# Kernel tuning notes

Measured on AMD Instinct MI355X. Metric: run time of the kernel, lower is better.

The kernel has to match this reference:

```python
import jax, jax.numpy as jnp
import numpy as np

N = 100_000   # nodes
E = 1_600_000 # edges
D = 128       # hidden/input dim
OUT = 32      # output dim
G = 512       # graphs in batch
L = 3         # conv layers


def setup_inputs() -> dict:
    key = jax.random.key(0)
    ks = jax.random.split(key, 12)
    s = 1.0 / np.sqrt(D)
    inp = {
        "x": jax.random.normal(ks[0], (N, D), jnp.float32),
        "edge_index": jax.random.randint(ks[1], (2, E), 0, N, dtype=jnp.int32),
        "batch": jnp.sort(jax.random.randint(ks[2], (N,), 0, G, dtype=jnp.int32)),
        "enc_W1": jax.random.normal(ks[3], (D, D), jnp.float32) * s,
        "enc_b1": jnp.zeros((D,), jnp.float32),
        "enc_W2": jax.random.normal(ks[4], (D, D), jnp.float32) * s,
        "enc_b2": jnp.zeros((D,), jnp.float32),
        "gcn_W": jax.random.normal(ks[5], (L, D, D), jnp.float32) * s,
        "gcn_b": jnp.zeros((L, D), jnp.float32),
        "dec_W1": jax.random.normal(ks[6], (D, D), jnp.float32) * s,
        "dec_b1": jnp.zeros((D,), jnp.float32),
        "dec_W2": jax.random.normal(ks[7], (D, OUT), jnp.float32) * s,
        "dec_b2": jnp.zeros((OUT,), jnp.float32),
        "num_graphs": G,
    }
    return inp


def reference(x, edge_index, batch, enc_W1, enc_b1, enc_W2, enc_b2,
              gcn_W, gcn_b, dec_W1, dec_b1, dec_W2, dec_b2, num_graphs):
    n = x.shape[0]
    src, dst = edge_index[0], edge_index[1]

    # ---- encoder MLP (Linear -> ReLU -> Linear -> ReLU) ----
    h = jax.nn.relu(x @ enc_W1 + enc_b1)
    h = jax.nn.relu(h @ enc_W2 + enc_b2)

    # ---- GCN normalization: D^{-1/2} (A + I) D^{-1/2}, degrees incl. self-loops ----
    deg = jax.ops.segment_sum(jnp.ones_like(src, dtype=h.dtype), dst, num_segments=n) + 1.0
    inv_sqrt = jax.lax.rsqrt(deg)           # [N]
    edge_coef = inv_sqrt[src] * inv_sqrt[dst]  # [E]
    self_coef = inv_sqrt * inv_sqrt            # [N]

    # ---- GCN conv layers ----
    for l in range(gcn_W.shape[0]):
        hw = h @ gcn_W[l]                                       # [N, D]
        msgs = hw[src] * edge_coef[:, None]                     # [E, D] gather
        agg = jax.ops.segment_sum(msgs, dst, num_segments=n)    # [N, D] scatter-add
        agg = agg + hw * self_coef[:, None]                     # self loops
        h = jax.nn.relu(agg + gcn_b[l])

    # ---- global add pool over graphs ----
    pooled = jax.ops.segment_sum(h, batch, num_segments=num_graphs)  # [G, D]

    # ---- decoder MLP ----
    out = jax.nn.relu(pooled @ dec_W1 + dec_b1)
    return out @ dec_W2 + dec_b2
```

## Files before the change

### kernel.cpp

```cpp
#include <hip/hip_runtime.h>

#define NNODES 100000
#define NEDGES 1600000
#define DIM    128
#define OUTD   32
#define NGRAPH 512

#define NBUCK2  256
#define BSHIFT  9
#define CAP     12288
#define EPB2    8192
#define SBLOCKS ((NEDGES + EPB2 - 1) / EPB2)
#define PREPBLK 160
#define NBUILD  ((NNODES + 511) / 512)
#define EBLK64  ((NNODES + 63) / 64)
#define AGGBLK  ((NNODES + 31) / 32)
#define NZERO   (NBUCK2 + NGRAPH * DIM)
#define ZBLOCKS ((NZERO + 511) / 512)

using bf16x8 = __attribute__((ext_vector_type(8))) short;
using f32x4  = __attribute__((ext_vector_type(4))) float;
using f32x2  = __attribute__((ext_vector_type(2))) float;

__device__ __forceinline__ short f2bf(float f) {
    unsigned u = __float_as_uint(f);
    unsigned r = (u + 0x7fff + ((u >> 16) & 1)) >> 16;
    return (short)r;
}
__device__ __forceinline__ float bf2f(short s) {
    return __uint_as_float(((unsigned)(unsigned short)s) << 16);
}

__device__ __forceinline__ uint2 bf8_to_fp8(bf16x8 t) {
    float f0 = bf2f(t[0]), f1 = bf2f(t[1]), f2 = bf2f(t[2]), f3 = bf2f(t[3]);
    float f4 = bf2f(t[4]), f5 = bf2f(t[5]), f6 = bf2f(t[6]), f7 = bf2f(t[7]);
    uint2 o;
    o.x = __builtin_amdgcn_cvt_pk_fp8_f32(f0, f1, 0, false);
    o.x = __builtin_amdgcn_cvt_pk_fp8_f32(f2, f3, o.x, true);
    o.y = __builtin_amdgcn_cvt_pk_fp8_f32(f4, f5, 0, false);
    o.y = __builtin_amdgcn_cvt_pk_fp8_f32(f6, f7, o.y, true);
    return o;
}

__global__ __launch_bounds__(512) void k_zero(int* __restrict__ gz)
{
    int idx = blockIdx.x * 512 + threadIdx.x;
    if (idx < NZERO) gz[idx] = 0;
}

__global__ __launch_bounds__(512) void k_scatter_prep(
    const int* __restrict__ src, const int* __restrict__ dst,
    int* __restrict__ gcur, unsigned* __restrict__ tmp,
    const float* __restrict__ eW1, const float* __restrict__ eW2,
    const float* __restrict__ gW, short* __restrict__ WT)
{
    const int tid = threadIdx.x;

    if (blockIdx.x >= SBLOCKS) {
        int idx = (blockIdx.x - SBLOCKS) * 512 + tid;
        int mat = idx >> 14, rem = idx & 16383;
        int k = rem >> 7, n = rem & 127;
        const float* sp = (mat == 0) ? eW1 : (mat == 1) ? eW2
                                           : (gW + (size_t)(mat - 2) * 16384);
        WT[(size_t)mat * 16384 + n * DIM + k] = f2bf(sp[k * DIM + n]);
        return;
    }

    __shared__ unsigned short rnk[EPB2];
    __shared__ int h[NBUCK2];
    __shared__ int gbase[NBUCK2];
    const int base = blockIdx.x * EPB2;
    if (tid < NBUCK2) h[tid] = 0;
    __syncthreads();
    #pragma unroll
    for (int it = 0; it < EPB2 / 512; ++it) {
        int e = base + it * 512 + tid;
        if (e < NEDGES) {
            int b = dst[e] >> BSHIFT;
            rnk[it * 512 + tid] = (unsigned short)atomicAdd(&h[b], 1);
        }
    }
    __syncthreads();
    if (tid < NBUCK2 && h[tid] > 0)
        gbase[tid] = tid * CAP + atomicAdd(&gcur[tid], h[tid]);
    __syncthreads();
    #pragma unroll
    for (int it = 0; it < EPB2 / 512; ++it) {
        int e = base + it * 512 + tid;
        if (e < NEDGES) {
            int d = dst[e], sv = src[e];
            int b = d >> BSHIFT;
            int pos = gbase[b] + rnk[it * 512 + tid];
            if (pos < (b + 1) * CAP)
                tmp[pos] = (unsigned)sv | ((unsigned)(d & 511) << 17);
        }
    }
}

__global__ __launch_bounds__(512, 6) void k_build_enc01(
    const unsigned* __restrict__ tmp, const int* __restrict__ gcur,
    int* __restrict__ row_off, int* __restrict__ cntA,
    float* __restrict__ inv, int* __restrict__ col,
    const float* __restrict__ x, const short* __restrict__ WT,
    const float* __restrict__ b1, const float* __restrict__ b2,
    short* __restrict__ hbuf, int M)
{
    __shared__ short As[64 * 128];
    __shared__ short Bs[128 * 128];

    const int tid = threadIdx.x;

    if (blockIdx.x < NBUILD) {
        int* hist = (int*)As;
        int* sc   = hist + 512;
        int* lcur = sc + 512;
        const int b     = blockIdx.x;
        const int tbase = b * CAP;
        const int cnt_b = min(gcur[b], CAP);
        hist[tid] = 0;
        __syncthreads();
        for (int i = tid; i < cnt_b; i += 512)
            atomicAdd(&hist[(tmp[tbase + i] >> 17) & 511], 1);
        __syncthreads();
        const int hv = hist[tid];
        sc[tid] = hv;
        __syncthreads();
        for (int off = 1; off < 512; off <<= 1) {
            int t = (tid >= off) ? sc[tid - off] : 0;
            __syncthreads();
            sc[tid] += t;
            __syncthreads();
        }
        const int start = tbase + sc[tid] - hv;
        lcur[tid] = start;
        const int node = b * 512 + tid;
        if (node < NNODES) {
            row_off[node] = start;
            cntA[node]    = hv;
            inv[node]     = rsqrtf((float)hv + 1.0f);
        }
        __syncthreads();
        for (int i = tid; i < cnt_b; i += 512) {
            unsigned t = tmp[tbase + i];
            int pos = atomicAdd(&lcur[(t >> 17) & 511], 1);
            col[pos] = (int)((t & 0x1FFFFu) << 7);
        }
        return;
    }

    const int m0 = (blockIdx.x - NBUILD) * 64;

    #pragma unroll
    for (int i = 0; i < 2; ++i) {
        int u = tid + i * 512;
        int row = u >> 4, c = u & 15;
        int gr = min(m0 + row, M - 1);
        const float4* sp = (const float4*)(x + (size_t)gr * DIM + (c << 3));
        float4 f0 = sp[0], f1 = sp[1];
        short t8[8] = { f2bf(f0.x), f2bf(f0.y), f2bf(f0.z), f2bf(f0.w),
                        f2bf(f1.x), f2bf(f1.y), f2bf(f1.z), f2bf(f1.w) };
        *(bf16x8*)&As[row * 128 + ((c ^ (row & 15)) << 3)] = *(bf16x8*)t8;
    }

    const int wave = tid >> 6, lane = tid & 63;
    const int ml = lane & 15, quad = lane >> 4;
    const int rw = wave >> 1;
    const int cw = wave & 1;

    #pragma unroll
    for (int mat = 0; mat < 2; ++mat) {
        if (mat > 0) __syncthreads();
        #pragma unroll
        for (int i = 0; i < 4; ++i) {
            int u = tid + i * 512;
            int n = u >> 4, c = u & 15;
            *(bf16x8*)&Bs[n * 128 + ((c ^ (n & 15)) << 3)] =
                *(const bf16x8*)(WT + (size_t)mat * 16384 + n * DIM + (c << 3));
        }
        __syncthreads();

        f32x4 acc[4] = {};
        const int arow = rw * 16 + ml;
        #pragma unroll
        for (int kk = 0; kk < 4; ++kk) {
            const int c = kk * 4 + quad;
            bf16x8 a = *(bf16x8*)&As[arow * 128 + ((c ^ (arow & 15)) << 3)];
            #pragma unroll
            for (int ni = 0; ni < 4; ++ni) {
                const int brow = (cw * 4 + ni) * 16 + ml;
                bf16x8 b = *(bf16x8*)&Bs[brow * 128 + ((c ^ (brow & 15)) << 3)];
                acc[ni] = __builtin_amdgcn_mfma_f32_16x16x32_bf16(a, b, acc[ni], 0, 0, 0);
            }
        }
        __syncthreads();

        #pragma unroll
        for (int ni = 0; ni < 4; ++ni) {
            const int colc = cw * 64 + ni * 16 + ml;
            const int cc = colc >> 3, w = colc & 7;
            #pragma unroll
            for (int r = 0; r < 4; ++r) {
                const int rowl = rw * 16 + quad * 4 + r;
                float v = acc[ni][r];
                v = fmaxf(v + ((mat == 0) ? b1[colc] : b2[colc]), 0.f);
                As[rowl * 128 + (((cc ^ (rowl & 15)) << 3) | w)] = f2bf(v);
            }
        }
    }
    __syncthreads();

    #pragma unroll
    for (int i = 0; i < 2; ++i) {
        int u = tid + i * 512;
        int row = u >> 4, c = u & 15;
        int gr = m0 + row;
        if (gr < M) {
            *(bf16x8*)(hbuf + (size_t)gr * DIM + (c << 3)) =
                *(bf16x8*)&As[row * 128 + ((c ^ (row & 15)) << 3)];
        }
    }
}

__global__ __launch_bounds__(512, 8) void k_enc2(
    const short* __restrict__ hbuf, const short* __restrict__ WT,
    const float* __restrict__ inv, unsigned char* __restrict__ g8)
{
    __shared__ short As[32 * 128];
    __shared__ short Bs[128 * 128];

    const int tid = threadIdx.x;
    const int m0  = blockIdx.x * 32;

    #pragma unroll
    for (int i = 0; i < 4; ++i) {
        int u = tid + i * 512;
        int n = u >> 4, c = u & 15;
        *(bf16x8*)&Bs[n * 128 + ((c ^ (n & 15)) << 3)] =
            *(const bf16x8*)(WT + n * DIM + (c << 3));
    }
    {
        int row = tid >> 4, c = tid & 15;
        *(bf16x8*)&As[row * 128 + ((c ^ (row & 15)) << 3)] =
            *(const bf16x8*)(hbuf + (size_t)(m0 + row) * DIM + (c << 3));
    }
    __syncthreads();

    const int wave = tid >> 6, lane = tid & 63;
    const int q  = lane >> 4, sl = lane & 15;
    const int mh = wave >> 2;
    const int nq = wave & 3;
    f32x4 acc[2] = {};
    #pragma unroll
    for (int kk = 0; kk < 4; ++kk) {
        const int c = kk * 4 + q;
        bf16x8 a = *(bf16x8*)&As[(mh * 16 + sl) * 128 + ((c ^ sl) << 3)];
        #pragma unroll
        for (int ni = 0; ni < 2; ++ni) {
            bf16x8 b = *(bf16x8*)&Bs[((nq * 2 + ni) * 16 + sl) * 128 + ((c ^ sl) << 3)];
            acc[ni] = __builtin_amdgcn_mfma_f32_16x16x32_bf16(a, b, acc[ni], 0, 0, 0);
        }
    }
    __syncthreads();

    #pragma unroll
    for (int ni = 0; ni < 2; ++ni) {
        const int colc = (nq * 2 + ni) * 16 + sl;
        const int cc = colc >> 3, cw = colc & 7;
        #pragma unroll
        for (int r = 0; r < 4; ++r) {
            const int rowl = mh * 16 + q * 4 + r;
            As[rowl * 128 + (((cc ^ (rowl & 15)) << 3) | cw)] =
                f2bf(acc[ni][r] * inv[m0 + rowl]);
        }
    }
    __syncthreads();

    {
        int row = tid >> 4, c = tid & 15;
        bf16x8 t = *(bf16x8*)&As[row * 128 + ((c ^ (row & 15)) << 3)];
        *(uint2*)(g8 + (size_t)(m0 + row) * DIM + (c << 3)) = bf8_to_fp8(t);
    }
}

#define GATHER_PIPELINE()                                                      \
    const int rs = row_off[node];                                              \
    const int re = rs + cntA[node];                                            \
    int j = rs;                                                                \
    {                                                                          \
        uint2 b0, b1_, b2_, b3_, b4_, b5_, b6_, b7_;                           \
        const bool hav = (j + 7 < re);                                         \
        if (hav) {                                                             \
            b0 = GLD(col[j]);     b1_ = GLD(col[j + 1]);                       \
            b2_ = GLD(col[j + 2]); b3_ = GLD(col[j + 3]);                      \
            b4_ = GLD(col[j + 4]); b5_ = GLD(col[j + 5]);                      \
            b6_ = GLD(col[j + 6]); b7_ = GLD(col[j + 7]);                      \
            j += 8;                                                            \
        }                                                                      \
        for (; j + 7 < re; j += 8) {                                           \
            uint2 n0 = GLD(col[j]);     uint2 n1 = GLD(col[j + 1]);            \
            uint2 n2 = GLD(col[j + 2]); uint2 n3 = GLD(col[j + 3]);            \
            uint2 n4 = GLD(col[j + 4]); uint2 n5 = GLD(col[j + 5]);            \
            uint2 n6 = GLD(col[j + 6]); uint2 n7 = GLD(col[j + 7]);            \
            ACC8(b0) ACC8(b1_) ACC8(b2_) ACC8(b3_)                             \
            ACC8(b4_) ACC8(b5_) ACC8(b6_) ACC8(b7_)                            \
            b0 = n0; b1_ = n1; b2_ = n2; b3_ = n3;                             \
            b4_ = n4; b5_ = n5; b6_ = n6; b7_ = n7;                            \
        }                                                                      \
        if (hav) {                                                             \
            ACC8(b0) ACC8(b1_) ACC8(b2_) ACC8(b3_)                             \
            ACC8(b4_) ACC8(b5_) ACC8(b6_) ACC8(b7_)                            \
        }                                                                      \
    }                                                                          \
    for (; j + 3 < re; j += 4) {                                               \
        uint2 v0 = GLD(col[j]);     uint2 v1 = GLD(col[j + 1]);                \
        uint2 v2 = GLD(col[j + 2]); uint2 v3 = GLD(col[j + 3]);                \
        ACC8(v0) ACC8(v1) ACC8(v2) ACC8(v3)                                    \
    }                                                                          \
    for (; j < re; ++j) {                                                      \
        uint2 v = GLD(col[j]);                                                 \
        ACC8(v)                                                                \
    }

__global__ __launch_bounds__(512, 8) void k_agg_gemm(
    const unsigned char* __restrict__ g8v, const int* __restrict__ row_off,
    const int* __restrict__ cntA, const int* __restrict__ col,
    const float* __restrict__ inv, const float* __restrict__ bias,
    const short* __restrict__ WT, unsigned char* __restrict__ g8o)
{
    __shared__ short As[32 * 128];
    __shared__ short Bs[128 * 128];

    const int tid = threadIdx.x;

    #pragma unroll
    for (int i = 0; i < 4; ++i) {
        int u = tid + i * 512;
        int n = u >> 4, c = u & 15;
        *(bf16x8*)&Bs[n * 128 + ((c ^ (n & 15)) << 3)] =
            *(const bf16x8*)(WT + n * DIM + (c << 3));
    }

    const int wave = tid >> 6, lane = tid & 63;
    const int q    = lane >> 4;
    const int sl   = lane & 15;
    const int sl8  = sl << 3;
    const int nl   = wave * 4 + q;
    const int m0   = blockIdx.x * 32;
    const int node = m0 + nl;

    f32x2 a01, a23, a45, a67;
    {
        uint2 us = *(const uint2*)(g8v + (size_t)node * 128 + sl8);
        a01 = __builtin_amdgcn_cvt_pk_f32_fp8(us.x, false);
        a23 = __builtin_amdgcn_cvt_pk_f32_fp8(us.x, true);
        a45 = __builtin_amdgcn_cvt_pk_f32_fp8(us.y, false);
        a67 = __builtin_amdgcn_cvt_pk_f32_fp8(us.y, true);
    }

    #define ACC8(v) \
        a01 += __builtin_amdgcn_cvt_pk_f32_fp8(v.x, false); \
        a23 += __builtin_amdgcn_cvt_pk_f32_fp8(v.x, true);  \
        a45 += __builtin_amdgcn_cvt_pk_f32_fp8(v.y, false); \
        a67 += __builtin_amdgcn_cvt_pk_f32_fp8(v.y, true);
    #define GLD(c) (*(const uint2*)(g8v + (size_t)(unsigned)((c) + sl8)))

    GATHER_PIPELINE()

    #undef ACC8
    #undef GLD

    const float scv = inv[node];
    const float4 bb0 = ((const float4*)bias)[sl * 2];
    const float4 bb1 = ((const float4*)bias)[sl * 2 + 1];
    short o[8];
    o[0] = f2bf(fmaxf(fmaf(a01[0], scv, bb0.x), 0.f));
    o[1] = f2bf(fmaxf(fmaf(a01[1], scv, bb0.y), 0.f));
    o[2] = f2bf(fmaxf(fmaf(a23[0], scv, bb0.z), 0.f));
    o[3] = f2bf(fmaxf(fmaf(a23[1], scv, bb0.w), 0.f));
    o[4] = f2bf(fmaxf(fmaf(a45[0], scv, bb1.x), 0.f));
    o[5] = f2bf(fmaxf(fmaf(a45[1], scv, bb1.y), 0.f));
    o[6] = f2bf(fmaxf(fmaf(a67[0], scv, bb1.z), 0.f));
    o[7] = f2bf(fmaxf(fmaf(a67[1], scv, bb1.w), 0.f));
    *(bf16x8*)&As[nl * 128 + ((sl ^ (nl & 15)) << 3)] = *(bf16x8*)o;
    __syncthreads();

    const int mh = wave >> 2;
    const int nq = wave & 3;
    f32x4 acc[2] = {};
    #pragma unroll
    for (int kk = 0; kk < 4; ++kk) {
        const int c = kk * 4 + q;
        bf16x8 a = *(bf16x8*)&As[(mh * 16 + sl) * 128 + ((c ^ sl) << 3)];
        #pragma unroll
        for (int ni = 0; ni < 2; ++ni) {
            bf16x8 b = *(bf16x8*)&Bs[((nq * 2 + ni) * 16 + sl) * 128 + ((c ^ sl) << 3)];
            acc[ni] = __builtin_amdgcn_mfma_f32_16x16x32_bf16(a, b, acc[ni], 0, 0, 0);
        }
    }
    __syncthreads();

    #pragma unroll
    for (int ni = 0; ni < 2; ++ni) {
        const int colc = (nq * 2 + ni) * 16 + sl;
        const int cc   = colc >> 3, cw = colc & 7;
        #pragma unroll
        for (int r = 0; r < 4; ++r) {
            const int rowl = mh * 16 + q * 4 + r;
            As[rowl * 128 + (((cc ^ (rowl & 15)) << 3) | cw)] =
                f2bf(acc[ni][r] * inv[m0 + rowl]);
        }
    }
    __syncthreads();

    {
        int row = tid >> 4, c = tid & 15;
        bf16x8 t = *(bf16x8*)&As[row * 128 + ((c ^ (row & 15)) << 3)];
        *(uint2*)(g8o + (size_t)(m0 + row) * DIM + (c << 3)) = bf8_to_fp8(t);
    }
}

__global__ __launch_bounds__(512) void k_agg_pool(
    const unsigned char* __restrict__ g8v, const int* __restrict__ row_off,
    const int* __restrict__ cntA, const int* __restrict__ col,
    const float* __restrict__ inv, const float* __restrict__ bias,
    const int* __restrict__ batch, float* __restrict__ pooled)
{
    __shared__ float Hs[32][132];
    __shared__ int sbatch[32];

    const int tid = threadIdx.x;
    const int wave = tid >> 6, lane = tid & 63;
    const int q    = lane >> 4;
    const int sl   = lane & 15;
    const int sl8  = sl << 3;
    const int nl   = wave * 4 + q;
    const int m0   = blockIdx.x * 32;
    const int node = m0 + nl;

    if (tid < 32) sbatch[tid] = batch[m0 + tid];

    f32x2 a01, a23, a45, a67;
    {
        uint2 us = *(const uint2*)(g8v + (size_t)node * 128 + sl8);
        a01 = __builtin_amdgcn_cvt_pk_f32_fp8(us.x, false);
        a23 = __builtin_amdgcn_cvt_pk_f32_fp8(us.x, true);
        a45 = __builtin_amdgcn_cvt_pk_f32_fp8(us.y, false);
        a67 = __builtin_amdgcn_cvt_pk_f32_fp8(us.y, true);
    }

    #define ACC8(v) \
        a01 += __builtin_amdgcn_cvt_pk_f32_fp8(v.x, false); \
        a23 += __builtin_amdgcn_cvt_pk_f32_fp8(v.x, true);  \
        a45 += __builtin_amdgcn_cvt_pk_f32_fp8(v.y, false); \
        a67 += __builtin_amdgcn_cvt_pk_f32_fp8(v.y, true);
    #define GLD(c) (*(const uint2*)(g8v + (size_t)(unsigned)((c) + sl8)))

    GATHER_PIPELINE()

    #undef ACC8
    #undef GLD

    const float scv = inv[node];
    const float4 bb0 = ((const float4*)bias)[sl * 2];
    const float4 bb1 = ((const float4*)bias)[sl * 2 + 1];
    float4 h0, h1;
    h0.x = fmaxf(fmaf(a01[0], scv, bb0.x), 0.f);
    h0.y = fmaxf(fmaf(a01[1], scv, bb0.y), 0.f);
    h0.z = fmaxf(fmaf(a23[0], scv, bb0.z), 0.f);
    h0.w = fmaxf(fmaf(a23[1], scv, bb0.w), 0.f);
    h1.x = fmaxf(fmaf(a45[0], scv, bb1.x), 0.f);
    h1.y = fmaxf(fmaf(a45[1], scv, bb1.y), 0.f);
    h1.z = fmaxf(fmaf(a67[0], scv, bb1.z), 0.f);
    h1.w = fmaxf(fmaf(a67[1], scv, bb1.w), 0.f);
    *(float4*)&Hs[nl][sl * 8]     = h0;
    *(float4*)&Hs[nl][sl * 8 + 4] = h1;
    __syncthreads();

    const int d   = tid & 127;
    const int grp = tid >> 7;
    float acc = 0.f;
    int cg = -1;
    #pragma unroll
    for (int i = 0; i < 8; ++i) {
        const int nn = grp * 8 + i;
        const int g  = sbatch[nn];
        if (g != cg) {
            if (cg >= 0) atomicAdd(pooled + (size_t)cg * DIM + d, acc);
            cg = g; acc = 0.f;
        }
        acc += Hs[nn][d];
    }
    atomicAdd(pooled + (size_t)cg * DIM + d, acc);
}

__global__ __launch_bounds__(512) void k_dec(
    const float* __restrict__ pooled, const float* __restrict__ W1,
    const float* __restrict__ b1, const float* __restrict__ W2,
    const float* __restrict__ b2, float* __restrict__ out)
{
    __shared__ float pbuf[8][128];
    __shared__ float tbuf[8][128];
    const int wave = threadIdx.x >> 6, lane = threadIdx.x & 63;
    const int g = blockIdx.x * 8 + wave;

    float2 pv = *(const float2*)(pooled + (size_t)g * DIM + lane * 2);
    pbuf[wave][lane * 2]     = pv.x;
    pbuf[wave][lane * 2 + 1] = pv.y;
    __syncthreads();

    float t0 = 0.f, t1 = 0.f;
    #pragma unroll 8
    for (int k = 0; k < DIM; ++k) {
        float pk = pbuf[wave][k];
        float2 w = *(const float2*)(W1 + (size_t)k * DIM + lane * 2);
        t0 = fmaf(pk, w.x, t0);
        t1 = fmaf(pk, w.y, t1);
    }
    tbuf[wave][lane * 2]     = fmaxf(t0 + b1[lane * 2],     0.f);
    tbuf[wave][lane * 2 + 1] = fmaxf(t1 + b1[lane * 2 + 1], 0.f);
    __syncthreads();

    const int c = lane & 31, hh = lane >> 5;
    float part = 0.f;
    #pragma unroll 8
    for (int kk = 0; kk < 64; ++kk) {
        int k = hh * 64 + kk;
        part = fmaf(tbuf[wave][k], W2[(size_t)k * OUTD + c], part);
    }
    float other = __shfl_xor(part, 32, 64);
    if (hh == 0)
        out[(size_t)g * OUTD + c] = part + other + b2[c];
}

extern "C" void kernel_launch(void* const* d_in, const int* in_sizes, int n_in,
                              void* d_out, int out_size, void* d_ws, size_t ws_size,
                              hipStream_t stream)
{
    const float* x      = (const float*)d_in[0];
    const int*   ei     = (const int*)d_in[1];
    const int*   batch  = (const int*)d_in[2];
    const float* enc_W1 = (const float*)d_in[3];
    const float* enc_b1 = (const float*)d_in[4];
    const float* enc_W2 = (const float*)d_in[5];
    const float* enc_b2 = (const float*)d_in[6];
    const float* gcn_W  = (const float*)d_in[7];
    const float* gcn_b  = (const float*)d_in[8];
    const float* dec_W1 = (const float*)d_in[9];
    const float* dec_b1 = (const float*)d_in[10];
    const float* dec_W2 = (const float*)d_in[11];
    const float* dec_b2 = (const float*)d_in[12];
    float* out = (float*)d_out;

    const int* src = ei;
    const int* dst = ei + NEDGES;

    char* p = (char*)d_ws;
    auto alloc = [&](size_t bytes) -> void* {
        void* r = (void*)p;
        p += (bytes + 255) & ~(size_t)255;
        return r;
    };
    int*           gcur   = (int*)          alloc((size_t)NBUCK2 * sizeof(int));
    float*         pooled = (float*)        alloc((size_t)NGRAPH * DIM * sizeof(float));
    unsigned char* g8a    = (unsigned char*)alloc((size_t)NNODES * DIM);
    unsigned char* g8b    = (unsigned char*)alloc((size_t)NNODES * DIM);
    short*         hbuf   = (short*)        alloc((size_t)NNODES * DIM * sizeof(short));
    float*         inv    = (float*)        alloc((size_t)NNODES * sizeof(float));
    int*           row_off= (int*)          alloc((size_t)NNODES * sizeof(int));
    int*           cntA   = (int*)          alloc((size_t)NNODES * sizeof(int));
    int*           col    = (int*)          alloc((size_t)NBUCK2 * CAP * sizeof(int));
    unsigned*      tmp    = (unsigned*)     alloc((size_t)NBUCK2 * CAP * sizeof(unsigned));
    short*         WT     = (short*)        alloc((size_t)5 * DIM * DIM * sizeof(short));

    k_zero<<<ZBLOCKS, 512, 0, stream>>>(gcur);

    k_scatter_prep<<<SBLOCKS + PREPBLK, 512, 0, stream>>>(
        src, dst, gcur, tmp, enc_W1, enc_W2, gcn_W, WT);

    k_build_enc01<<<NBUILD + EBLK64, 512, 0, stream>>>(
        tmp, gcur, row_off, cntA, inv, col,
        x, WT, enc_b1, enc_b2, hbuf, NNODES);

    k_enc2<<<AGGBLK, 512, 0, stream>>>(hbuf, WT + 2 * 16384, inv, g8a);

    k_agg_gemm<<<AGGBLK, 512, 0, stream>>>(g8a, row_off, cntA, col, inv,
                                           gcn_b,       WT + 3 * 16384, g8b);
    k_agg_gemm<<<AGGBLK, 512, 0, stream>>>(g8b, row_off, cntA, col, inv,
                                           gcn_b + 128, WT + 4 * 16384, g8a);
    k_agg_pool<<<AGGBLK, 512, 0, stream>>>(g8a, row_off, cntA, col, inv,
                                           gcn_b + 256, batch, pooled);

    k_dec <<<NGRAPH / 8, 512, 0, stream>>>(pooled, dec_W1, dec_b1,
                                           dec_W2, dec_b2, out);
}
```

Baseline: 293.5 us.

## Enlarge enc2 GEMM tile to 128 rows and cache dst in LDS during scatter

The second encoder GEMM now processes 128 rows per block instead of 32, so the 32 KB bf16 weight tile loaded into LDS is reused across four times as many rows. Each wave computes a 4x2 grid of MFMA tiles, and the tail block is handled with clamped loads and guarded stores. The scatter-prep kernel halves its edges per block and keeps each dst value in shared memory, so the second pass no longer reloads dst from global memory. In exchange there are fewer, larger enc2 blocks with more LDS and more accumulator registers per block, and twice as many scatter blocks contending on the global bucket counters.

After: 293.9 us. Within noise of the previous version (+0.1%).

```diff
diff --git a/kernel.cpp b/kernel.cpp
--- a/kernel.cpp
+++ b/kernel.cpp
@@ -9,11 +9,12 @@
 #define NBUCK2  256
 #define BSHIFT  9
 #define CAP     12288
-#define EPB2    8192
+#define EPB2    4096
 #define SBLOCKS ((NEDGES + EPB2 - 1) / EPB2)
 #define PREPBLK 160
 #define NBUILD  ((NNODES + 511) / 512)
 #define EBLK64  ((NNODES + 63) / 64)
+#define EBLK128 ((NNODES + 127) / 128)
 #define AGGBLK  ((NNODES + 31) / 32)
 #define NZERO   (NBUCK2 + NGRAPH * DIM)
 #define ZBLOCKS ((NZERO + 511) / 512)
@@ -67,6 +68,7 @@
     }
 
     __shared__ unsigned short rnk[EPB2];
+    __shared__ unsigned       eds[EPB2];
     __shared__ int h[NBUCK2];
     __shared__ int gbase[NBUCK2];
     const int base = blockIdx.x * EPB2;
@@ -76,8 +78,9 @@
     for (int it = 0; it < EPB2 / 512; ++it) {
         int e = base + it * 512 + tid;
         if (e < NEDGES) {
-            int b = dst[e] >> BSHIFT;
-            rnk[it * 512 + tid] = (unsigned short)atomicAdd(&h[b], 1);
+            unsigned d = (unsigned)dst[e];
+            eds[it * 512 + tid] = d;
+            rnk[it * 512 + tid] = (unsigned short)atomicAdd(&h[d >> BSHIFT], 1);
         }
     }
     __syncthreads();
@@ -88,11 +91,12 @@
     for (int it = 0; it < EPB2 / 512; ++it) {
         int e = base + it * 512 + tid;
         if (e < NEDGES) {
-            int d = dst[e], sv = src[e];
+            unsigned d = eds[it * 512 + tid];
+            int sv = src[e];
             int b = d >> BSHIFT;
             int pos = gbase[b] + rnk[it * 512 + tid];
             if (pos < (b + 1) * CAP)
-                tmp[pos] = (unsigned)sv | ((unsigned)(d & 511) << 17);
+                tmp[pos] = (unsigned)sv | ((d & 511) << 17);
         }
     }
 }
@@ -221,15 +225,15 @@
     }
 }
 
-__global__ __launch_bounds__(512, 8) void k_enc2(
+__global__ __launch_bounds__(512, 4) void k_enc2(
     const short* __restrict__ hbuf, const short* __restrict__ WT,
-    const float* __restrict__ inv, unsigned char* __restrict__ g8)
-{
-    __shared__ short As[32 * 128];
+    const float* __restrict__ inv, unsigned char* __restrict__ g8, int M)
+{
+    __shared__ short As[128 * 128];
     __shared__ short Bs[128 * 128];
 
     const int tid = threadIdx.x;
-    const int m0  = blockIdx.x * 32;
+    const int m0  = blockIdx.x * 128;
 
     #pragma unroll
     for (int i = 0; i < 4; ++i) {
@@ -238,10 +242,13 @@
         *(bf16x8*)&Bs[n * 128 + ((c ^ (n & 15)) << 3)] =
             *(const bf16x8*)(WT + n * DIM + (c << 3));
     }
-    {
-        int row = tid >> 4, c = tid & 15;
+    #pragma unroll
+    for (int i = 0; i < 4; ++i) {
+        int u = tid + i * 512;
+        int row = u >> 4, c = u & 15;
+        int gr = min(m0 + row, M - 1);
         *(bf16x8*)&As[row * 128 + ((c ^ (row & 15)) << 3)] =
-            *(const bf16x8*)(hbuf + (size_t)(m0 + row) * DIM + (c << 3));
+            *(const bf16x8*)(hbuf + (size_t)gr * DIM + (c << 3));
     }
     __syncthreads();
 
@@ -249,36 +256,47 @@
     const int q  = lane >> 4, sl = lane & 15;
     const int mh = wave >> 2;
     const int nq = wave & 3;
-    f32x4 acc[2] = {};
+    f32x4 acc[4][2] = {};
     #pragma unroll
     for (int kk = 0; kk < 4; ++kk) {
         const int c = kk * 4 + q;
-        bf16x8 a = *(bf16x8*)&As[(mh * 16 + sl) * 128 + ((c ^ sl) << 3)];
+        bf16x8 b0 = *(bf16x8*)&Bs[((nq * 2 + 0) * 16 + sl) * 128 + ((c ^ sl) << 3)];
+        bf16x8 b1v = *(bf16x8*)&Bs[((nq * 2 + 1) * 16 + sl) * 128 + ((c ^ sl) << 3)];
+        #pragma unroll
+        for (int r4 = 0; r4 < 4; ++r4) {
+            const int arow = (mh * 4 + r4) * 16 + sl;
+            bf16x8 a = *(bf16x8*)&As[arow * 128 + ((c ^ sl) << 3)];
+            acc[r4][0] = __builtin_amdgcn_mfma_f32_16x16x32_bf16(a, b0, acc[r4][0], 0, 0, 0);
+            acc[r4][1] = __builtin_amdgcn_mfma_f32_16x16x32_bf16(a, b1v, acc[r4][1], 0, 0, 0);
+        }
+    }
+    __syncthreads();
+
+    #pragma unroll
+    for (int r4 = 0; r4 < 4; ++r4) {
         #pragma unroll
         for (int ni = 0; ni < 2; ++ni) {
-            bf16x8 b = *(bf16x8*)&Bs[((nq * 2 + ni) * 16 + sl) * 128 + ((c ^ sl) << 3)];
-            acc[ni] = __builtin_amdgcn_mfma_f32_16x16x32_bf16(a, b, acc[ni], 0, 0, 0);
-        }
-    }
-    __syncthreads();
-
-    #pragma unroll
-    for (int ni = 0; ni < 2; ++ni) {
-        const int colc = (nq * 2 + ni) * 16 + sl;
-        const int cc = colc >> 3, cw = colc & 7;
-        #pragma unroll
-        for (int r = 0; r < 4; ++r) {
-            const int rowl = mh * 16 + q * 4 + r;
-            As[rowl * 128 + (((cc ^ (rowl & 15)) << 3) | cw)] =
-                f2bf(acc[ni][r] * inv[m0 + rowl]);
-        }
-    }
-    __syncthreads();
-
-    {
-        int row = tid >> 4, c = tid & 15;
-        bf16x8 t = *(bf16x8*)&As[row * 128 + ((c ^ (row & 15)) << 3)];
-        *(uint2*)(g8 + (size_t)(m0 + row) * DIM + (c << 3)) = bf8_to_fp8(t);
+            const int colc = (nq * 2 + ni) * 16 + sl;
+            const int cc = colc >> 3, cw = colc & 7;
+            #pragma unroll
+            for (int r = 0; r < 4; ++r) {
+                const int rowl = (mh * 4 + r4) * 16 + q * 4 + r;
+                As[rowl * 128 + (((cc ^ (rowl & 15)) << 3) | cw)] =
+                    f2bf(acc[r4][ni][r] * inv[min(m0 + rowl, M - 1)]);
+            }
+        }
+    }
+    __syncthreads();
+
+    #pragma unroll
+    for (int i = 0; i < 4; ++i) {
+        int u = tid + i * 512;
+        int row = u >> 4, c = u & 15;
+        int gr = m0 + row;
+        if (gr < M) {
+            bf16x8 t = *(bf16x8*)&As[row * 128 + ((c ^ (row & 15)) << 3)];
+            *(uint2*)(g8 + (size_t)gr * DIM + (c << 3)) = bf8_to_fp8(t);
+        }
     }
 }
 
@@ -581,7 +599,7 @@
         tmp, gcur, row_off, cntA, inv, col,
         x, WT, enc_b1, enc_b2, hbuf, NNODES);
 
-    k_enc2<<<AGGBLK, 512, 0, stream>>>(hbuf, WT + 2 * 16384, inv, g8a);
+    k_enc2<<<EBLK128, 512, 0, stream>>>(hbuf, WT + 2 * 16384, inv, g8a, NNODES);
 
     k_agg_gemm<<<AGGBLK, 512, 0, stream>>>(g8a, row_off, cntA, col, inv,
                                            gcn_b,       WT + 3 * 16384, g8b);
```
